# Kernel optimization log

Hardware: AMD Instinct MI355X
Metric: run time of the kernel (lower is better)

## Reference

```python
import jax, jax.numpy as jnp
import numpy as np

N = 100000   # nodes
E = 1600000  # edges (avg degree 16)
D = 30       # in channels
H = 4        # attention heads
C = 30       # per-head out channels
EPS = 1e-5
NEG_SLOPE = 0.2


def setup_inputs() -> dict:
    ks = jax.random.split(jax.random.key(0), 12)
    s = 0.1
    return {
        "h": jax.random.normal(ks[0], (N, D), jnp.float32),
        "edge_index": jax.random.randint(ks[1], (2, E), 0, N),
        "edge_weight": jax.random.uniform(ks[2], (E,), jnp.float32),
        "bn_gamma": jnp.ones((D,), jnp.float32),
        "bn_beta": jnp.zeros((D,), jnp.float32),
        "W": jax.random.normal(ks[3], (D, H * C), jnp.float32) * s,
        "att_src": jax.random.normal(ks[4], (H, C), jnp.float32) * s,
        "att_dst": jax.random.normal(ks[5], (H, C), jnp.float32) * s,
        "att_edge": jax.random.normal(ks[6], (H, C), jnp.float32) * s,
        "W_edge": jax.random.normal(ks[7], (1, H * C), jnp.float32) * s,
        "bias": jnp.zeros((C,), jnp.float32),
        "fc1_w": jax.random.normal(ks[8], (C, C), jnp.float32) * s,
        "fc1_b": jnp.zeros((C,), jnp.float32),
        "fc2_w": jax.random.normal(ks[9], (C, C), jnp.float32) * s,
        "fc2_b": jnp.zeros((C,), jnp.float32),
        "fc3_w": jax.random.normal(ks[10], (C, C), jnp.float32) * s,
        "fc3_b": jnp.zeros((C,), jnp.float32),
    }


def reference(h, edge_index, edge_weight, bn_gamma, bn_beta, W, att_src, att_dst,
              att_edge, W_edge, bias, fc1_w, fc1_b, fc2_w, fc2_b, fc3_w, fc3_b):
    n = h.shape[0]
    # BatchNorm1d, training-mode batch statistics (biased variance)
    mu = h.mean(0)
    var = ((h - mu) ** 2).mean(0)
    hn = (h - mu) * jax.lax.rsqrt(var + EPS) * bn_gamma + bn_beta

    # GATConv with add_self_loops=True; self-loop edge_attr = mean edge weight
    # (PyG fill_value='mean' default)
    loop = jnp.arange(n)
    src = jnp.concatenate([edge_index[0], loop])
    dst = jnp.concatenate([edge_index[1], loop])
    ew = jnp.concatenate([edge_weight, jnp.full((n,), edge_weight.mean(), h.dtype)])

    x = (hn @ W).reshape(n, H, C)                    # [N,H,C] shared src/dst lin
    a_src = (x * att_src).sum(-1)                    # [N,H]
    a_dst = (x * att_dst).sum(-1)                    # [N,H]
    e = (ew[:, None] * W_edge[0]).reshape(-1, H, C)  # [E2,H,C] lin_edge (no bias)
    a_edge = (e * att_edge).sum(-1)                  # [E2,H]

    alpha = jax.nn.leaky_relu(a_src[src] + a_dst[dst] + a_edge, NEG_SLOPE)
    # scatter-softmax over incoming edges of each destination node
    m = jax.ops.segment_max(alpha, dst, num_segments=n)
    ex = jnp.exp(alpha - m[dst])
    den = jax.ops.segment_sum(ex, dst, num_segments=n)
    alpha = ex / (den[dst] + 1e-16)                  # [E2,H]

    out = jax.ops.segment_sum(x[src] * alpha[:, :, None], dst, num_segments=n)
    out = out.mean(1) + bias                         # concat=False -> head mean

    out = jax.nn.relu(out)
    out = jax.nn.relu(out @ fc1_w.T + fc1_b)
    out = jax.nn.relu(out @ fc2_w.T + fc2_b)
    return out @ fc3_w.T + fc3_b
```

## Files before the change

kernel.cpp:

```cpp
#include <hip/hip_runtime.h>
#include <hip/hip_fp16.h>

#define N_NODES 100000
#define N_EDGES 1600000
#define D_IN 30
#define H_HEADS 4
#define C_OUT 30
#define EPSV 1e-5f
#define NEG 0.2f
#define MAXDEG 48
#define NPB 64
#define NBUCK 256
#define BUCK_NODES 391
#define SLICE_CAP 48
#define EPB 4096
#define BIN_BLOCKS ((N_EDGES + EPB - 1) / EPB)
#define STATS_BLOCKS 224
#define X_BLOCKS ((N_NODES + NPB - 1) / NPB)
#define NODE_BLOCKS (N_NODES / 16)

#define OFF_XH    0
#define OFF_ADST  6400000
#define OFF_PAR   6800000
#define OFF_DEG   6804096
#define OFF_STATS 6904256
#define OFF_BCNTG 6904320
#define OFF_ADJ   7004416
#define OFF_GBUF  11804416

__device__ __forceinline__ float hb2f(unsigned int bits) {
    __half_raw r; r.x = (unsigned short)bits;
    return __half2float(*reinterpret_cast<__half*>(&r));
}

__global__ __launch_bounds__(512) void k_bin(const int* __restrict__ ei,
                                             const float* __restrict__ ew,
                                             const float* __restrict__ h,
                                             unsigned int* __restrict__ bcnt_g,
                                             uint2* __restrict__ gbuf,
                                             float* __restrict__ stats) {
    int t = threadIdx.x;
    if (blockIdx.x < BIN_BLOCKS) {
        __shared__ int bcnt[NBUCK];
        if (t < NBUCK) bcnt[t] = 0;
        __syncthreads();
        int blk = blockIdx.x;
        int j0 = blk * EPB + t;
#pragma unroll
        for (int r = 0; r < 8; ++r) {
            int j = j0 + r * 512;
            if (j < N_EDGES) {
                int s = __builtin_nontemporal_load(ei + j);
                int d = __builtin_nontemporal_load(ei + N_EDGES + j);
                float w = __builtin_nontemporal_load(ew + j);
                __half hv = __float2half_rn(w);
                unsigned short hb = *reinterpret_cast<unsigned short*>(&hv);
                unsigned lo = ((unsigned)s << 15) | (unsigned)(hb & 0x7FFFu);
                int b = d / BUCK_NODES;
                int rank = atomicAdd(&bcnt[b], 1);
                if (rank < SLICE_CAP)
                    gbuf[((size_t)b * BIN_BLOCKS + blk) * SLICE_CAP + rank] =
                        make_uint2(lo, (unsigned)d);
            }
        }
        __syncthreads();
        if (t < NBUCK) bcnt_g[(size_t)blk * NBUCK + t] = (unsigned)bcnt[t];
        return;
    }
    __shared__ float ls[61];
    if (t < 61) ls[t] = 0.f;
    __syncthreads();
    float s[D_IN], q[D_IN];
#pragma unroll
    for (int d = 0; d < D_IN; ++d) { s[d] = 0.f; q[d] = 0.f; }
    int idx0 = (blockIdx.x - BIN_BLOCKS) * 512 + t;
    int stride = STATS_BLOCKS * 512;
    for (int r = idx0; r < N_NODES; r += stride) {
        const float* row = h + r * D_IN;
#pragma unroll
        for (int d = 0; d < D_IN; ++d) { float v = row[d]; s[d] += v; q[d] += v * v; }
    }
    float es = 0.f;
    for (int i = idx0; i < N_EDGES; i += stride) es += ew[i];
#pragma unroll
    for (int d = 0; d < D_IN; ++d) {
        for (int off = 32; off; off >>= 1) {
            s[d] += __shfl_down(s[d], off);
            q[d] += __shfl_down(q[d], off);
        }
    }
    for (int off = 32; off; off >>= 1) es += __shfl_down(es, off);
    if ((t & 63) == 0) {
#pragma unroll
        for (int d = 0; d < D_IN; ++d) { atomicAdd(&ls[d], s[d]); atomicAdd(&ls[30 + d], q[d]); }
        atomicAdd(&ls[60], es);
    }
    __syncthreads();
    if (t < 61) atomicAdd(&stats[t], ls[t]);
}

__global__ __launch_bounds__(256) void k_bx(const unsigned int* __restrict__ bcnt_g,
                                            const uint2* __restrict__ gbuf,
                                            unsigned int* __restrict__ adj,
                                            int* __restrict__ deg,
                                            const float* __restrict__ h,
                                            const float* __restrict__ W,
                                            const float* __restrict__ Wedge,
                                            const float* __restrict__ att_edge,
                                            const float* __restrict__ att_src,
                                            const float* __restrict__ att_dst,
                                            const float* __restrict__ gamma,
                                            const float* __restrict__ beta,
                                            const float* __restrict__ stats,
                                            float* __restrict__ par,
                                            unsigned int* __restrict__ xh,
                                            float* __restrict__ adst) {
    __shared__ __align__(16) unsigned char smem[38416];
    int t = threadIdx.x;
    if (blockIdx.x < 2 * NBUCK) {
        unsigned* rows = (unsigned*)smem;
        int* cnt = (int*)(smem + 37632);
        int bb = blockIdx.x;
        int b = bb >> 1, half = bb & 1;
        int lo = b * BUCK_NODES + half * 196;
        int span = half ? (BUCK_NODES - 196) : 196;
        int lim = N_NODES - lo; if (lim > span) lim = span; if (lim < 0) lim = 0;
        for (int i = t; i < 196; i += 256) cnt[i] = 0;
        __syncthreads();
        const uint2* brec = gbuf + (size_t)b * BIN_BLOCKS * SLICE_CAP;
        int totslots = BIN_BLOCKS * SLICE_CAP;
        for (int i = t; i < totslots; i += 256) {
            int sl = i / SLICE_CAP;
            int r = i - sl * SLICE_CAP;
            unsigned c = bcnt_g[(size_t)sl * NBUCK + b];
            if (r < (int)c) {
                uint2 rec = brec[i];
                int li = (int)rec.y - lo;
                if (li >= 0 && li < lim) {
                    int p = atomicAdd(&cnt[li], 1);
                    if (p < MAXDEG) rows[li * MAXDEG + p] = rec.x;
                }
            }
        }
        __syncthreads();
        int tot = lim * MAXDEG;
        for (int i = t; i < tot; i += 256) {
            int li = i / MAXDEG;
            int p = i - li * MAXDEG;
            if (p < cnt[li]) adj[(size_t)lo * MAXDEG + i] = rows[i];
        }
        for (int i = t; i < lim; i += 256) { int c = cnt[i]; deg[lo + i] = (c > MAXDEG) ? MAXDEG : c; }
        return;
    }
    float* W2s = (float*)smem;
    float* hs  = (float*)(smem + 14400);
    float* psd = (float*)(smem + 22080);
    float* cq  = (float*)(smem + 23040);
    float* b2s = (float*)(smem + 23072);
    float* scs = (float*)(smem + 23552);
    float* shs = (float*)(smem + 23672);
    int bx = blockIdx.x - 2 * NBUCK;
    if (t < D_IN) {
        float mu = stats[t] * (1.f / N_NODES);
        float var = stats[30 + t] * (1.f / N_NODES) - mu * mu;
        float inv = 1.f / sqrtf(var + EPSV);
        float sc = gamma[t] * inv;
        scs[t] = sc; shs[t] = beta[t] - mu * sc;
    }
    __syncthreads();
    for (int i = t; i < 3600; i += 256) W2s[i] = scs[i / 120] * W[i];
    if (t >= 128 && t < 248) {
        int c = t - 128;
        float b = 0.f;
#pragma unroll
        for (int d = 0; d < D_IN; ++d) b = fmaf(shs[d], W[d * 120 + c], b);
        b2s[c] = b;
    }
    if (bx == 0 && t >= 248 && t < 252) {
        int hh = t - 248;
        float k = 0.f;
        for (int c = 0; c < 30; ++c) k = fmaf(Wedge[hh * 30 + c], att_edge[hh * 30 + c], k);
        par[64 + hh] = k;
    }
    if (bx == 0 && t == 252) par[68] = stats[60] * (1.f / N_EDGES);
    __syncthreads();
    int base = bx * NPB;
    int cnt2 = N_NODES - base; if (cnt2 > NPB) cnt2 = NPB;
    if (t < 240) {
        int d = t >> 3, q = t & 7, hh = q & 3;
        const float* att = (q < 4) ? att_src : att_dst;
        float sum = 0.f;
#pragma unroll
        for (int c = 0; c < 30; ++c) sum = fmaf(W2s[d * 120 + hh * 30 + c], att[hh * 30 + c], sum);
        psd[t] = sum;
    }
    if (t >= 240 && t < 248) {
        int q = t - 240, hh = q & 3;
        const float* att = (q < 4) ? att_src : att_dst;
        float sum = 0.f;
#pragma unroll
        for (int c = 0; c < 30; ++c) sum = fmaf(b2s[hh * 30 + c], att[hh * 30 + c], sum);
        cq[q] = sum;
    }
    for (int i = t; i < cnt2 * 30; i += 256) hs[i] = h[(size_t)base * 30 + i];
    __syncthreads();
    const float2* W2p = (const float2*)W2s;
    int total = cnt2 * 60;
    for (int o = t; o < total; o += 256) {
        int node = o / 60, p = o - node * 60;
        const float* hrow = hs + node * 30;
        float ax = b2s[2 * p], ay = b2s[2 * p + 1];
        const float2* Wp = W2p + p;
#pragma unroll
        for (int d = 0; d < 30; ++d) {
            float hv = hrow[d];
            float2 w = Wp[d * 60];
            ax = fmaf(hv, w.x, ax);
            ay = fmaf(hv, w.y, ay);
        }
        __half2 pk = __float22half2_rn(make_float2(ax, ay));
        int hh = p / 15, j = p - hh * 15;
        xh[(size_t)(base + node) * 64 + hh * 16 + j] = *reinterpret_cast<unsigned int*>(&pk);
    }
    for (int v = t; v < cnt2 * 8; v += 256) {
        int node = v >> 3, q = v & 7;
        const float* hrow = hs + node * 30;
        float sum = cq[q];
#pragma unroll
        for (int d = 0; d < 30; ++d) sum = fmaf(hrow[d], psd[d * 8 + q], sum);
        int n = base + node;
        if (q < 4) xh[(size_t)n * 64 + q * 16 + 15] = __float_as_uint(sum);
        else       adst[n * H_HEADS + (q - 4)] = sum;
    }
}

__global__ __launch_bounds__(256) void k_node(const uint4* __restrict__ xh4,
                                              const float* __restrict__ adst,
                                              const float* __restrict__ par,
                                              const int* __restrict__ deg,
                                              const unsigned int* __restrict__ adj,
                                              const float* __restrict__ bias,
                                              const float* __restrict__ fc1w,
                                              const float* __restrict__ fc1b,
                                              const float* __restrict__ fc2w,
                                              const float* __restrict__ fc2b,
                                              const float* __restrict__ fc3w,
                                              const float* __restrict__ fc3b,
                                              float* __restrict__ out) {
    __shared__ float Ws[3][900];
    __shared__ float Bs[3][30];
    __shared__ float bias_s[32];
    __shared__ float tb[16 * 32];
    int t = threadIdx.x;
    {
        const float4* s0 = (const float4*)fc1w;
        const float4* s1 = (const float4*)fc2w;
        const float4* s2 = (const float4*)fc3w;
        for (int i = t; i < 225; i += 256) {
            *(float4*)&Ws[0][i * 4] = s0[i];
            *(float4*)&Ws[1][i * 4] = s1[i];
            *(float4*)&Ws[2][i * 4] = s2[i];
        }
    }
    if (t < 30) { Bs[0][t] = fc1b[t]; Bs[1][t] = fc2b[t]; Bs[2][t] = fc3b[t]; }
    if (t < 32) bias_s[t] = (t < 30) ? bias[t] : 0.f;
    __syncthreads();

    int l = t & 63;
    int k = l & 15;
    int wv = t >> 6;
    int q = (l >> 4) & 3;
    int nl = wv * 4 + q;
    int n = blockIdx.x * 16 + nl;
    int h = k >> 2;
    int asl_b = (((l & 48) | (k & 12) | 3) << 2);
    int pb4 = (l & 48) << 2;

    float kh = par[64 + h];
    float ew_mean = par[68];
    float adn = adst[n * H_HEADS + h];

    int dn = min(deg[n], MAXDEG);
    int dmax = dn;
    dmax = max(dmax, __shfl_xor(dmax, 16));
    dmax = max(dmax, __shfl_xor(dmax, 32));

    const unsigned int* arow = adj + (size_t)n * MAXDEG;
    unsigned int aw0 = arow[k];
    unsigned int aw1 = arow[16 + k];
    unsigned int aw2 = arow[32 + k];

    uint4 rw = xh4[(unsigned)n * 16u + (unsigned)k];
    float asn = __uint_as_float((unsigned)__builtin_amdgcn_ds_bpermute(asl_b, (int)rw.w));
    float z = fmaf(ew_mean, kh, adn) + asn;
    z = fmaxf(z, NEG * z);
    float e0 = __expf(z);
    float den = e0;
    float2 x0 = __half22float2(*(const __half2*)&rw.x);
    float2 x1 = __half22float2(*(const __half2*)&rw.y);
    float2 x2 = __half22float2(*(const __half2*)&rw.z);
    float2 x3 = __half22float2(*(const __half2*)&rw.w);
    float2 a0 = make_float2(e0 * x0.x, e0 * x0.y);
    float2 a1 = make_float2(e0 * x1.x, e0 * x1.y);
    float2 a2 = make_float2(e0 * x2.x, e0 * x2.y);
    float2 a3 = make_float2(e0 * x3.x, e0 * x3.y);

#pragma unroll 2
    for (int u = 0; u < dmax; ++u) {
        unsigned int aw = (u < 16) ? aw0 : ((u < 32) ? aw1 : aw2);
        unsigned int ewd = (unsigned)__builtin_amdgcn_ds_bpermute(pb4 + ((u & 15) << 2), (int)aw);
        bool valid = (u < dn);
        unsigned s = valid ? (ewd >> 15) : (unsigned)n;
        uint4 r = xh4[s * 16u + (unsigned)k];
        float w = hb2f(ewd & 0x7FFFu);
        float as_ = __uint_as_float((unsigned)__builtin_amdgcn_ds_bpermute(asl_b, (int)r.w));
        float zz = fmaf(w, kh, adn) + as_;
        zz = fmaxf(zz, NEG * zz);
        float ee = __expf(zz);
        ee = valid ? ee : 0.f;
        den += ee;
        float2 y0 = __half22float2(*(const __half2*)&r.x);
        float2 y1 = __half22float2(*(const __half2*)&r.y);
        float2 y2 = __half22float2(*(const __half2*)&r.z);
        float2 y3 = __half22float2(*(const __half2*)&r.w);
        a0.x = fmaf(ee, y0.x, a0.x); a0.y = fmaf(ee, y0.y, a0.y);
        a1.x = fmaf(ee, y1.x, a1.x); a1.y = fmaf(ee, y1.y, a1.y);
        a2.x = fmaf(ee, y2.x, a2.x); a2.y = fmaf(ee, y2.y, a2.y);
        a3.x = fmaf(ee, y3.x, a3.x); a3.y = fmaf(ee, y3.y, a3.y);
    }

    float rden = 0.25f / (den + 1e-16f);
    a0.x *= rden; a0.y *= rden; a1.x *= rden; a1.y *= rden;
    a2.x *= rden; a2.y *= rden; a3.x *= rden; a3.y *= rden;

    a0.x += __shfl_xor(a0.x, 4); a0.y += __shfl_xor(a0.y, 4);
    a1.x += __shfl_xor(a1.x, 4); a1.y += __shfl_xor(a1.y, 4);
    a2.x += __shfl_xor(a2.x, 4); a2.y += __shfl_xor(a2.y, 4);
    a3.x += __shfl_xor(a3.x, 4); a3.y += __shfl_xor(a3.y, 4);
    a0.x += __shfl_xor(a0.x, 8); a0.y += __shfl_xor(a0.y, 8);
    a1.x += __shfl_xor(a1.x, 8); a1.y += __shfl_xor(a1.y, 8);
    a2.x += __shfl_xor(a2.x, 8); a2.y += __shfl_xor(a2.y, 8);
    a3.x += __shfl_xor(a3.x, 8); a3.y += __shfl_xor(a3.y, 8);

    if ((k & 12) == 0) {
        int ch = k * 8;
        float v0 = fmaxf(a0.x + bias_s[ch + 0], 0.f);
        float v1 = fmaxf(a0.y + bias_s[ch + 1], 0.f);
        float v2 = fmaxf(a1.x + bias_s[ch + 2], 0.f);
        float v3 = fmaxf(a1.y + bias_s[ch + 3], 0.f);
        float v4 = fmaxf(a2.x + bias_s[ch + 4], 0.f);
        float v5 = fmaxf(a2.y + bias_s[ch + 5], 0.f);
        float v6 = fmaxf(a3.x + bias_s[ch + 6], 0.f);
        float v7 = fmaxf(a3.y + bias_s[ch + 7], 0.f);
        float* p = tb + nl * 32 + ch;
        *(float4*)p       = make_float4(v0, v1, v2, v3);
        *(float4*)(p + 4) = make_float4(v4, v5, v6, v7);
    }
    __syncthreads();

    int base16 = blockIdx.x * 16;
    for (int lay = 0; lay < 3; ++lay) {
        float y[2];
#pragma unroll
        for (int j = 0; j < 2; ++j) {
            int i = t + j * 256;
            int nd = i >> 5, c = i & 31;
            y[j] = 0.f;
            if (c < 30) {
                float acc = Bs[lay][c];
                const float* Wl = &Ws[lay][c * 30];
                const float* tr = &tb[nd * 32];
#pragma unroll
                for (int cc = 0; cc < 30; ++cc) acc = fmaf(tr[cc], Wl[cc], acc);
                y[j] = (lay < 2) ? fmaxf(acc, 0.f) : acc;
            }
        }
        __syncthreads();
#pragma unroll
        for (int j = 0; j < 2; ++j) {
            int i = t + j * 256;
            int nd = i >> 5, c = i & 31;
            if (c < 30) {
                if (lay < 2) tb[nd * 32 + c] = y[j];
                else out[(size_t)(base16 + nd) * 30 + c] = y[j];
            }
        }
        if (lay < 2) __syncthreads();
    }
}

extern "C" void kernel_launch(void* const* d_in, const int* in_sizes, int n_in,
                              void* d_out, int out_size, void* d_ws, size_t ws_size,
                              hipStream_t stream) {
    const float* h        = (const float*)d_in[0];
    const int*   ei       = (const int*)d_in[1];
    const float* ew       = (const float*)d_in[2];
    const float* gamma    = (const float*)d_in[3];
    const float* beta     = (const float*)d_in[4];
    const float* W        = (const float*)d_in[5];
    const float* att_src  = (const float*)d_in[6];
    const float* att_dst  = (const float*)d_in[7];
    const float* att_edge = (const float*)d_in[8];
    const float* Wedge    = (const float*)d_in[9];
    const float* bias     = (const float*)d_in[10];
    const float* fc1w     = (const float*)d_in[11];
    const float* fc1b     = (const float*)d_in[12];
    const float* fc2w     = (const float*)d_in[13];
    const float* fc2b     = (const float*)d_in[14];
    const float* fc3w     = (const float*)d_in[15];
    const float* fc3b     = (const float*)d_in[16];

    float*        ws     = (float*)d_ws;
    unsigned int* xh     = (unsigned int*)(ws + OFF_XH);
    float*        adstb  = ws + OFF_ADST;
    float*        par    = ws + OFF_PAR;
    float*        stats  = ws + OFF_STATS;
    int*          deg    = (int*)(ws + OFF_DEG);
    unsigned int* bcnt_g = (unsigned int*)(ws + OFF_BCNTG);
    unsigned int* adj    = (unsigned int*)(ws + OFF_ADJ);
    uint2*        gbuf   = (uint2*)(ws + OFF_GBUF);
    float*        out    = (float*)d_out;

    hipMemsetAsync(stats, 0, 64 * 4, stream);

    k_bin<<<BIN_BLOCKS + STATS_BLOCKS, 512, 0, stream>>>(ei, ew, h, bcnt_g, gbuf, stats);
    k_bx<<<2 * NBUCK + X_BLOCKS, 256, 0, stream>>>(bcnt_g, gbuf, adj, deg, h, W, Wedge,
                                                   att_edge, att_src, att_dst,
                                                   gamma, beta, stats, par, xh, adstb);
    k_node<<<NODE_BLOCKS, 256, 0, stream>>>((const uint4*)xh, adstb, par, deg, adj,
                                            bias, fc1w, fc1b, fc2w, fc2b, fc3w, fc3b, out);
}
```

Baseline: 194.6 us.

## Sort nodes by degree within buckets to balance per-block gather work

```diff
diff --git a/kernel.cpp b/kernel.cpp
--- a/kernel.cpp
+++ b/kernel.cpp
@@ -27,6 +27,7 @@
 #define OFF_BCNTG 6904320
 #define OFF_ADJ   7004416
 #define OFF_GBUF  11804416
+#define OFF_PERM  21413632
 
 __device__ __forceinline__ float hb2f(unsigned int bits) {
     __half_raw r; r.x = (unsigned short)bits;
@@ -103,6 +104,7 @@
                                             const uint2* __restrict__ gbuf,
                                             unsigned int* __restrict__ adj,
                                             int* __restrict__ deg,
+                                            int* __restrict__ perm,
                                             const float* __restrict__ h,
                                             const float* __restrict__ W,
                                             const float* __restrict__ Wedge,
@@ -115,17 +117,20 @@
                                             float* __restrict__ par,
                                             unsigned int* __restrict__ xh,
                                             float* __restrict__ adst) {
-    __shared__ __align__(16) unsigned char smem[38416];
+    __shared__ __align__(16) unsigned char smem[38816];
     int t = threadIdx.x;
     if (blockIdx.x < 2 * NBUCK) {
         unsigned* rows = (unsigned*)smem;
         int* cnt = (int*)(smem + 37632);
+        int* hist = (int*)(smem + 38416);
+        int* pfx  = (int*)(smem + 38612);
         int bb = blockIdx.x;
         int b = bb >> 1, half = bb & 1;
         int lo = b * BUCK_NODES + half * 196;
         int span = half ? (BUCK_NODES - 196) : 196;
         int lim = N_NODES - lo; if (lim > span) lim = span; if (lim < 0) lim = 0;
         for (int i = t; i < 196; i += 256) cnt[i] = 0;
+        if (t < 49) hist[t] = 0;
         __syncthreads();
         const uint2* brec = gbuf + (size_t)b * BIN_BLOCKS * SLICE_CAP;
         int totslots = BIN_BLOCKS * SLICE_CAP;
@@ -149,7 +154,22 @@
             int p = i - li * MAXDEG;
             if (p < cnt[li]) adj[(size_t)lo * MAXDEG + i] = rows[i];
         }
-        for (int i = t; i < lim; i += 256) { int c = cnt[i]; deg[lo + i] = (c > MAXDEG) ? MAXDEG : c; }
+        for (int i = t; i < lim; i += 256) {
+            int c = cnt[i]; c = (c > MAXDEG) ? MAXDEG : c;
+            deg[lo + i] = c;
+            atomicAdd(&hist[c], 1);
+        }
+        __syncthreads();
+        if (t == 0) {
+            int acc = 0;
+            for (int kk = MAXDEG; kk >= 0; --kk) { pfx[kk] = acc; acc += hist[kk]; }
+        }
+        __syncthreads();
+        for (int i = t; i < lim; i += 256) {
+            int c = cnt[i]; c = (c > MAXDEG) ? MAXDEG : c;
+            int r = atomicAdd(&pfx[c], 1);
+            perm[lo + r] = lo + i;
+        }
         return;
     }
     float* W2s = (float*)smem;
@@ -239,6 +259,7 @@
                                               const float* __restrict__ par,
                                               const int* __restrict__ deg,
                                               const unsigned int* __restrict__ adj,
+                                              const int* __restrict__ perm,
                                               const float* __restrict__ bias,
                                               const float* __restrict__ fc1w,
                                               const float* __restrict__ fc1b,
@@ -251,6 +272,7 @@
     __shared__ float Bs[3][30];
     __shared__ float bias_s[32];
     __shared__ float tb[16 * 32];
+    __shared__ int nids[16];
     int t = threadIdx.x;
     {
         const float4* s0 = (const float4*)fc1w;
@@ -271,7 +293,8 @@
     int wv = t >> 6;
     int q = (l >> 4) & 3;
     int nl = wv * 4 + q;
-    int n = blockIdx.x * 16 + nl;
+    int n = perm[blockIdx.x * 16 + nl];
+    if (k == 0) nids[nl] = n;
     int h = k >> 2;
     int asl_b = (((l & 48) | (k & 12) | 3) << 2);
     int pb4 = (l & 48) << 2;
@@ -287,8 +310,9 @@
 
     const unsigned int* arow = adj + (size_t)n * MAXDEG;
     unsigned int aw0 = arow[k];
-    unsigned int aw1 = arow[16 + k];
-    unsigned int aw2 = arow[32 + k];
+    unsigned int aw1 = 0, aw2 = 0;
+    if (dmax > 16) aw1 = arow[16 + k];
+    if (dmax > 32) aw2 = arow[32 + k];
 
     uint4 rw = xh4[(unsigned)n * 16u + (unsigned)k];
     float asn = __uint_as_float((unsigned)__builtin_amdgcn_ds_bpermute(asl_b, (int)rw.w));
@@ -358,7 +382,6 @@
     }
     __syncthreads();
 
-    int base16 = blockIdx.x * 16;
     for (int lay = 0; lay < 3; ++lay) {
         float y[2];
 #pragma unroll
@@ -382,7 +405,7 @@
             int nd = i >> 5, c = i & 31;
             if (c < 30) {
                 if (lay < 2) tb[nd * 32 + c] = y[j];
-                else out[(size_t)(base16 + nd) * 30 + c] = y[j];
+                else out[(size_t)nids[nd] * 30 + c] = y[j];
             }
         }
         if (lay < 2) __syncthreads();
@@ -419,14 +442,15 @@
     unsigned int* bcnt_g = (unsigned int*)(ws + OFF_BCNTG);
     unsigned int* adj    = (unsigned int*)(ws + OFF_ADJ);
     uint2*        gbuf   = (uint2*)(ws + OFF_GBUF);
+    int*          perm   = (int*)(ws + OFF_PERM);
     float*        out    = (float*)d_out;
 
     hipMemsetAsync(stats, 0, 64 * 4, stream);
 
     k_bin<<<BIN_BLOCKS + STATS_BLOCKS, 512, 0, stream>>>(ei, ew, h, bcnt_g, gbuf, stats);
-    k_bx<<<2 * NBUCK + X_BLOCKS, 256, 0, stream>>>(bcnt_g, gbuf, adj, deg, h, W, Wedge,
-                                                   att_edge, att_src, att_dst,
+    k_bx<<<2 * NBUCK + X_BLOCKS, 256, 0, stream>>>(bcnt_g, gbuf, adj, deg, perm, h, W,
+                                                   Wedge, att_edge, att_src, att_dst,
                                                    gamma, beta, stats, par, xh, adstb);
-    k_node<<<NODE_BLOCKS, 256, 0, stream>>>((const uint4*)xh, adstb, par, deg, adj,
+    k_node<<<NODE_BLOCKS, 256, 0, stream>>>((const uint4*)xh, adstb, par, deg, adj, perm,
                                             bias, fc1w, fc1b, fc2w, fc2b, fc3w, fc3b, out);
 }
```

Measured after the change: 185.8 us. 1.05x faster.
